# Optimization experiments

Measured on AMD Instinct MI355X. Metric: run time of the kernel, lower is better.

The kernel has to match this reference:

```python
import jax, jax.numpy as jnp
import numpy as np

N_EMBD = 384
NUM_HEADS = 6
HEAD_SIZE = 64
B, T = 64, 256


def setup_inputs() -> dict:
    key = jax.random.key(0)
    ks = jax.random.split(key, 6)
    s = 0.02
    x = jax.random.normal(ks[0], (B, T, N_EMBD), dtype=jnp.float32)
    # per-head projection weights, stored as [H, in, out] so y = x @ W
    Wq = jax.random.normal(ks[1], (NUM_HEADS, N_EMBD, HEAD_SIZE), dtype=jnp.float32) * s
    Wk = jax.random.normal(ks[2], (NUM_HEADS, N_EMBD, HEAD_SIZE), dtype=jnp.float32) * s
    Wv = jax.random.normal(ks[3], (NUM_HEADS, N_EMBD, HEAD_SIZE), dtype=jnp.float32) * s
    Wp = jax.random.normal(ks[4], (NUM_HEADS * HEAD_SIZE, N_EMBD), dtype=jnp.float32) * s
    bp = jax.random.normal(ks[5], (N_EMBD,), dtype=jnp.float32) * s
    return {"x": x, "Wq": Wq, "Wk": Wk, "Wv": Wv, "Wp": Wp, "bp": bp}


def reference(x, Wq, Wk, Wv, Wp, bp):
    # x: [B,T,C]; W{q,k,v}: [H,C,D]; dropout is identity (eval mode)
    Bb, Tt, _ = x.shape
    q = jnp.einsum('btc,hcd->bhtd', x, Wq)
    k = jnp.einsum('btc,hcd->bhtd', x, Wk)
    v = jnp.einsum('btc,hcd->bhtd', x, Wv)
    scale = HEAD_SIZE ** -0.5
    scores = jnp.einsum('bhtd,bhsd->bhts', q, k) * scale  # [B,H,T,T]
    causal = jnp.tril(jnp.ones((Tt, Tt), dtype=bool))
    scores = jnp.where(causal, scores, jnp.finfo(scores.dtype).min)
    attn = jax.nn.softmax(scores, axis=-1)
    out = jnp.einsum('bhts,bhsd->bhtd', attn, v)  # [B,H,T,D]
    out = out.transpose(0, 2, 1, 3).reshape(Bb, Tt, NUM_HEADS * HEAD_SIZE)
    return out @ Wp + bp
```

## Files before the change

### kernel.cpp

```cpp
#include <hip/hip_runtime.h>
#include <stdint.h>

#define B_  64
#define T_  256
#define C_  384
#define H_  6
#define D_  64
#define NTOK (B_*T_)

typedef float f32x4 __attribute__((ext_vector_type(4)));
typedef short s16x8 __attribute__((ext_vector_type(8)));

__device__ __forceinline__ unsigned short f2bf(float f) {
    unsigned int u;
    __builtin_memcpy(&u, &f, 4);
    u = u + 0x7FFFu + ((u >> 16) & 1u);
    return (unsigned short)(u >> 16);
}

__device__ __forceinline__ void async_copy16(const unsigned short* g, unsigned short* l) {
    __builtin_amdgcn_global_load_lds(
        (const __attribute__((address_space(1))) unsigned int*)g,
        (__attribute__((address_space(3))) unsigned int*)l, 16, 0, 0);
}

__global__ __launch_bounds__(256) void transpose_weights(
    const float* __restrict__ Wq, const float* __restrict__ Wk,
    const float* __restrict__ Wv, const float* __restrict__ Wp,
    unsigned short* __restrict__ W3, unsigned short* __restrict__ WTp) {
    __shared__ float tile[32][33];
    int z = blockIdx.y;
    const float* in;
    unsigned short* out;
    int R, Cc;
    if (z < 18) {
        int proj = z / 6, h = z % 6;
        const float* Wsrc = proj == 0 ? Wq : (proj == 1 ? Wk : Wv);
        in = Wsrc + h * C_ * D_;
        out = W3 + (size_t)(h * 192 + proj * 64) * C_;
        R = C_; Cc = D_;
    } else {
        in = Wp; out = WTp; R = C_; Cc = C_;
    }
    int tilesC = Cc / 32;
    int tilesR = R / 32;
    int bx = blockIdx.x;
    if (bx >= tilesC * tilesR) return;
    int tr = bx / tilesC, tc = bx % tilesC;
    int tx = threadIdx.x & 31;
    int ty8 = threadIdx.x >> 5;
    int gx = tc * 32 + tx;
#pragma unroll
    for (int i = 0; i < 4; i++) {
        int gy = tr * 32 + ty8 + i * 8;
        tile[ty8 + i * 8][tx] = in[gy * Cc + gx];
    }
    __syncthreads();
#pragma unroll
    for (int i = 0; i < 4; i++) {
        int oy = tc * 32 + ty8 + i * 8;
        int ox = tr * 32 + tx;
        out[oy * R + ox] = f2bf(tile[tx][ty8 + i * 8]);
    }
}

__global__ __launch_bounds__(512, 2) void fused_attn(
    const float* __restrict__ X, const unsigned short* __restrict__ W3,
    unsigned short* __restrict__ Ows) {
    __shared__ alignas(16) unsigned short smem[67584];
    unsigned short* Wc     = smem;
    unsigned short* q_lds  = smem + 18432;
    unsigned short* k_lds  = q_lds + 16384;
    unsigned short* vT_lds = k_lds + 16384;

    int bh = blockIdx.x;
    int h = bh >> 6, b = bh & 63;
    int tid = threadIdx.x;
    int w = tid >> 6, lane = tid & 63;
    int n16 = lane & 15, q4 = lane >> 4;
    const int jt[2] = {w, 15 - w};

    const unsigned short* W3h = W3 + (size_t)h * 192 * C_;
    const float* xb = X + (size_t)b * T_ * C_;

    f32x4 acc[2][12];
#pragma unroll
    for (int i = 0; i < 2; i++)
#pragma unroll
        for (int j = 0; j < 12; j++) acc[i][j] = (f32x4){0.f, 0.f, 0.f, 0.f};

    for (int kc = 0; kc < 4; kc++) {
        int ko = kc * 96;
        float4 a0[2][3], a1[2][3];
#pragma unroll
        for (int mi = 0; mi < 2; mi++)
#pragma unroll
            for (int ks = 0; ks < 3; ks++) {
                const float* ap = xb + (size_t)(jt[mi] * 16 + n16) * C_ + ko + ks * 32 + q4 * 8;
                a0[mi][ks] = *reinterpret_cast<const float4*>(ap);
                a1[mi][ks] = *reinterpret_cast<const float4*>(ap + 4);
            }
        if (kc) __syncthreads();
#pragma unroll
        for (int i = 0; i < 5; i++) {
            int sb = i * 512 + w * 64;
            if (sb < 2304) {
                int L = sb + lane;
                int row = L / 12;
                int c = L % 12;
                int ks = c >> 2;
                int q4g = (c & 3) ^ (row & 3);
                async_copy16(W3h + (size_t)row * C_ + ko + ks * 32 + q4g * 8,
                             Wc + (size_t)sb * 8);
            }
        }
        __syncthreads();
#pragma unroll
        for (int ks = 0; ks < 3; ks++) {
            s16x8 af[2];
#pragma unroll
            for (int mi = 0; mi < 2; mi++) {
                float4 lo = a0[mi][ks], hi = a1[mi][ks];
                s16x8 a;
                a[0] = (short)f2bf(lo.x); a[1] = (short)f2bf(lo.y);
                a[2] = (short)f2bf(lo.z); a[3] = (short)f2bf(lo.w);
                a[4] = (short)f2bf(hi.x); a[5] = (short)f2bf(hi.y);
                a[6] = (short)f2bf(hi.z); a[7] = (short)f2bf(hi.w);
                af[mi] = a;
            }
#pragma unroll
            for (int ni = 0; ni < 12; ni++) {
                int row = ni * 16 + n16;
                int cp = ks * 4 + (q4 ^ (row & 3));
                s16x8 bf = *reinterpret_cast<const s16x8*>(&Wc[row * 96 + cp * 8]);
                if (ni < 8) {
                    acc[0][ni] = __builtin_amdgcn_mfma_f32_16x16x32_bf16(bf, af[0], acc[0][ni], 0, 0, 0);
                    acc[1][ni] = __builtin_amdgcn_mfma_f32_16x16x32_bf16(bf, af[1], acc[1][ni], 0, 0, 0);
                } else {
                    acc[0][ni] = __builtin_amdgcn_mfma_f32_16x16x32_bf16(af[0], bf, acc[0][ni], 0, 0, 0);
                    acc[1][ni] = __builtin_amdgcn_mfma_f32_16x16x32_bf16(af[1], bf, acc[1][ni], 0, 0, 0);
                }
            }
        }
    }
#pragma unroll
    for (int mi = 0; mi < 2; mi++) {
        int tile = jt[mi];
#pragma unroll
        for (int ni = 0; ni < 12; ni++) {
            ushort4 pk;
            pk.x = f2bf(acc[mi][ni][0]); pk.y = f2bf(acc[mi][ni][1]);
            pk.z = f2bf(acc[mi][ni][2]); pk.w = f2bf(acc[mi][ni][3]);
            if (ni < 8) {
                int t = tile * 16 + n16;
                int cp = (2 * (ni & 3) + (q4 >> 1)) ^ (n16 & 7);
                unsigned short* dst = (ni < 4) ? q_lds : k_lds;
                *reinterpret_cast<ushort4*>(&dst[t * 64 + cp * 8 + (q4 & 1) * 4]) = pk;
            } else {
                int d = (ni - 8) * 16 + n16;
                int cp = (tile * 2 + (q4 >> 1)) ^ (d & 7);
                *reinterpret_cast<ushort4*>(&vT_lds[d * 256 + cp * 8 + (q4 & 1) * 4]) = pk;
            }
        }
    }
    __syncthreads();

    unsigned short* pw_base = smem + w * 1280;
    const f32x4 zero4 = (f32x4){0.f, 0.f, 0.f, 0.f};

#pragma unroll
    for (int tt = 0; tt < 2; tt++) {
        int j = jt[tt];
        int t0 = j * 16;
        int tq = t0 + n16;
        s16x8 qa0 = *reinterpret_cast<const s16x8*>(&q_lds[tq * 64 + ((q4 ^ (n16 & 7)) * 8)]);
        s16x8 qa1 = *reinterpret_cast<const s16x8*>(&q_lds[tq * 64 + (((q4 + 4) ^ (n16 & 7)) * 8)]);

        f32x4 o[4];
        float l_lane[4];
#pragma unroll
        for (int i = 0; i < 4; i++) o[i] = zero4;
#pragma unroll
        for (int r = 0; r < 4; r++) l_lane[r] = 0.f;

        int nch = j / 2 + 1;
        for (int c = 0; c < nch; c++) {
            int s0 = c * 32;
            bool bAct = (s0 + 16) < (t0 + 16);
            int r0 = s0 + n16, r1 = s0 + 16 + n16;
            s16x8 k00 = *reinterpret_cast<const s16x8*>(&k_lds[r0 * 64 + ((q4 ^ (r0 & 7)) * 8)]);
            s16x8 k01 = *reinterpret_cast<const s16x8*>(&k_lds[r0 * 64 + (((q4 + 4) ^ (r0 & 7)) * 8)]);
            f32x4 sv0 = __builtin_amdgcn_mfma_f32_16x16x32_bf16(qa0, k00, zero4, 0, 0, 0);
            sv0 = __builtin_amdgcn_mfma_f32_16x16x32_bf16(qa1, k01, sv0, 0, 0, 0);
            f32x4 sv1 = zero4;
            if (bAct) {
                s16x8 k10 = *reinterpret_cast<const s16x8*>(&k_lds[r1 * 64 + ((q4 ^ (r1 & 7)) * 8)]);
                s16x8 k11 = *reinterpret_cast<const s16x8*>(&k_lds[r1 * 64 + (((q4 + 4) ^ (r1 & 7)) * 8)]);
                sv1 = __builtin_amdgcn_mfma_f32_16x16x32_bf16(qa0, k10, zero4, 0, 0, 0);
                sv1 = __builtin_amdgcn_mfma_f32_16x16x32_bf16(qa1, k11, sv1, 0, 0, 0);
            }
            unsigned short* pw = pw_base + (c & 1) * 640;
#pragma unroll
            for (int r = 0; r < 4; r++) {
                int t = t0 + q4 * 4 + r;
                float pA = (s0 + n16 <= t) ? __expf(sv0[r] * 0.125f) : 0.f;
                float pB = (bAct && (s0 + 16 + n16 <= t)) ? __expf(sv1[r] * 0.125f) : 0.f;
                l_lane[r] += pA + pB;
                pw[(q4 * 4 + r) * 40 + n16] = f2bf(pA);
                pw[(q4 * 4 + r) * 40 + 16 + n16] = f2bf(pB);
            }
            s16x8 pa = *reinterpret_cast<const s16x8*>(&pw[n16 * 40 + q4 * 8]);
#pragma unroll
            for (int dt = 0; dt < 4; dt++) {
                int d = dt * 16 + n16;
                int jp = (c * 4 + q4) ^ (d & 7);
                s16x8 vf = *reinterpret_cast<const s16x8*>(&vT_lds[d * 256 + jp * 8]);
                o[dt] = __builtin_amdgcn_mfma_f32_16x16x32_bf16(pa, vf, o[dt], 0, 0, 0);
            }
        }

        float linv[4];
#pragma unroll
        for (int r = 0; r < 4; r++) {
            float l = l_lane[r];
            l += __shfl_xor(l, 1);
            l += __shfl_xor(l, 2);
            l += __shfl_xor(l, 4);
            l += __shfl_xor(l, 8);
            linv[r] = 1.0f / l;
        }
#pragma unroll
        for (int dt = 0; dt < 4; dt++) {
            int col = h * 64 + dt * 16 + n16;
#pragma unroll
            for (int r = 0; r < 4; r++)
                Ows[(size_t)(b * T_ + t0 + q4 * 4 + r) * C_ + col] = f2bf(o[dt][r] * linv[r]);
        }
    }
}

__global__ __launch_bounds__(256) void gemm_out(
    const unsigned short* __restrict__ A, const unsigned short* __restrict__ WTp,
    const float* __restrict__ bp, float* __restrict__ out) {
    __shared__ alignas(16) unsigned short Bt[6 * 128 * 32];
    int m0 = blockIdx.x * 128;
    int n0 = blockIdx.y * 128;
    int tid = threadIdx.x;
    int w = tid >> 6, lane = tid & 63;
    int n16 = lane & 15, q4 = lane >> 4;

    f32x4 acc[2][8];
#pragma unroll
    for (int i = 0; i < 2; i++)
#pragma unroll
        for (int j = 0; j < 8; j++) acc[i][j] = (f32x4){0.f, 0.f, 0.f, 0.f};

    const unsigned short* a_base[2];
#pragma unroll
    for (int mi = 0; mi < 2; mi++)
        a_base[mi] = A + (size_t)(m0 + w * 32 + mi * 16 + n16) * C_ + q4 * 8;

    for (int half = 0; half < 2; half++) {
        int ko = half * 192;
        s16x8 af[2][6];
#pragma unroll
        for (int mi = 0; mi < 2; mi++)
#pragma unroll
            for (int ks = 0; ks < 6; ks++)
                af[mi][ks] = *reinterpret_cast<const s16x8*>(a_base[mi] + ko + ks * 32);
        if (half) __syncthreads();
#pragma unroll
        for (int i = 0; i < 12; i++) {
            int L = w * 768 + i * 64 + lane;
            int kstep = L >> 9;
            int rem = L & 511;
            int row = rem >> 2;
            int j = (rem & 3) ^ (row & 3);
            async_copy16(WTp + (size_t)(n0 + row) * C_ + ko + kstep * 32 + j * 8,
                         Bt + (size_t)(w * 768 + i * 64) * 8);
        }
        __syncthreads();
#pragma unroll
        for (int ks = 0; ks < 6; ks++) {
            s16x8 bf[8];
#pragma unroll
            for (int ni = 0; ni < 8; ni++) {
                int row = ni * 16 + n16;
                int jp = q4 ^ (row & 3);
                bf[ni] = *reinterpret_cast<const s16x8*>(&Bt[ks * 4096 + row * 32 + jp * 8]);
            }
#pragma unroll
            for (int mi = 0; mi < 2; mi++)
#pragma unroll
                for (int ni = 0; ni < 8; ni++)
                    acc[mi][ni] = __builtin_amdgcn_mfma_f32_16x16x32_bf16(
                        bf[ni], af[mi][ks], acc[mi][ni], 0, 0, 0);
        }
    }

#pragma unroll
    for (int mi = 0; mi < 2; mi++) {
        int tr = m0 + w * 32 + mi * 16 + n16;
#pragma unroll
        for (int ni = 0; ni < 8; ni++) {
            int c0 = n0 + ni * 16 + q4 * 4;
            float4 bias = *reinterpret_cast<const float4*>(&bp[c0]);
            float4 res;
            res.x = acc[mi][ni][0] + bias.x;
            res.y = acc[mi][ni][1] + bias.y;
            res.z = acc[mi][ni][2] + bias.z;
            res.w = acc[mi][ni][3] + bias.w;
            *reinterpret_cast<float4*>(&out[(size_t)tr * C_ + c0]) = res;
        }
    }
}

extern "C" void kernel_launch(void* const* d_in, const int* in_sizes, int n_in,
                              void* d_out, int out_size, void* d_ws, size_t ws_size,
                              hipStream_t stream) {
    const float* x  = (const float*)d_in[0];
    const float* Wq = (const float*)d_in[1];
    const float* Wk = (const float*)d_in[2];
    const float* Wv = (const float*)d_in[3];
    const float* Wp = (const float*)d_in[4];
    const float* bp = (const float*)d_in[5];
    float* out = (float*)d_out;

    char* ws = (char*)d_ws;
    size_t off = 0;
    auto alloc = [&](size_t bytes) -> unsigned short* {
        unsigned short* p = (unsigned short*)(ws + off);
        off += (bytes + 255) & ~(size_t)255;
        return p;
    };
    unsigned short* W3  = alloc((size_t)H_ * 192 * C_ * 2);
    unsigned short* WTp = alloc((size_t)C_ * C_ * 2);
    unsigned short* Ows = alloc((size_t)NTOK * C_ * 2);

    transpose_weights<<<dim3(144, 19), dim3(256), 0, stream>>>(
        Wq, Wk, Wv, Wp, W3, WTp);
    fused_attn<<<dim3(B_ * H_), dim3(512), 0, stream>>>(x, W3, Ows);
    gemm_out<<<dim3(128, 3), dim3(256), 0, stream>>>(Ows, WTp, bp, out);
}
```

Measured before the change: 149.8 us.

## Double fused attention block to 16 waves with one query tile per wave

```diff
diff --git a/kernel.cpp b/kernel.cpp
--- a/kernel.cpp
+++ b/kernel.cpp
@@ -64,7 +64,7 @@
     }
 }
 
-__global__ __launch_bounds__(512, 2) void fused_attn(
+__global__ __launch_bounds__(1024, 4) void fused_attn(
     const float* __restrict__ X, const unsigned short* __restrict__ W3,
     unsigned short* __restrict__ Ows) {
     __shared__ alignas(16) unsigned short smem[67584];
@@ -78,32 +78,28 @@
     int tid = threadIdx.x;
     int w = tid >> 6, lane = tid & 63;
     int n16 = lane & 15, q4 = lane >> 4;
-    const int jt[2] = {w, 15 - w};
+    const int j = (w & 1) ? (15 - (w >> 1)) : (w >> 1);
 
     const unsigned short* W3h = W3 + (size_t)h * 192 * C_;
     const float* xb = X + (size_t)b * T_ * C_;
 
-    f32x4 acc[2][12];
-#pragma unroll
-    for (int i = 0; i < 2; i++)
-#pragma unroll
-        for (int j = 0; j < 12; j++) acc[i][j] = (f32x4){0.f, 0.f, 0.f, 0.f};
+    f32x4 acc[12];
+#pragma unroll
+    for (int i = 0; i < 12; i++) acc[i] = (f32x4){0.f, 0.f, 0.f, 0.f};
 
     for (int kc = 0; kc < 4; kc++) {
         int ko = kc * 96;
-        float4 a0[2][3], a1[2][3];
-#pragma unroll
-        for (int mi = 0; mi < 2; mi++)
-#pragma unroll
-            for (int ks = 0; ks < 3; ks++) {
-                const float* ap = xb + (size_t)(jt[mi] * 16 + n16) * C_ + ko + ks * 32 + q4 * 8;
-                a0[mi][ks] = *reinterpret_cast<const float4*>(ap);
-                a1[mi][ks] = *reinterpret_cast<const float4*>(ap + 4);
-            }
+        float4 a0[3], a1[3];
+#pragma unroll
+        for (int ks = 0; ks < 3; ks++) {
+            const float* ap = xb + (size_t)(j * 16 + n16) * C_ + ko + ks * 32 + q4 * 8;
+            a0[ks] = *reinterpret_cast<const float4*>(ap);
+            a1[ks] = *reinterpret_cast<const float4*>(ap + 4);
+        }
         if (kc) __syncthreads();
 #pragma unroll
-        for (int i = 0; i < 5; i++) {
-            int sb = i * 512 + w * 64;
+        for (int i = 0; i < 3; i++) {
+            int sb = i * 1024 + w * 64;
             if (sb < 2304) {
                 int L = sb + lane;
                 int row = L / 12;
@@ -117,60 +113,47 @@
         __syncthreads();
 #pragma unroll
         for (int ks = 0; ks < 3; ks++) {
-            s16x8 af[2];
-#pragma unroll
-            for (int mi = 0; mi < 2; mi++) {
-                float4 lo = a0[mi][ks], hi = a1[mi][ks];
-                s16x8 a;
-                a[0] = (short)f2bf(lo.x); a[1] = (short)f2bf(lo.y);
-                a[2] = (short)f2bf(lo.z); a[3] = (short)f2bf(lo.w);
-                a[4] = (short)f2bf(hi.x); a[5] = (short)f2bf(hi.y);
-                a[6] = (short)f2bf(hi.z); a[7] = (short)f2bf(hi.w);
-                af[mi] = a;
-            }
+            float4 lo = a0[ks], hi = a1[ks];
+            s16x8 af;
+            af[0] = (short)f2bf(lo.x); af[1] = (short)f2bf(lo.y);
+            af[2] = (short)f2bf(lo.z); af[3] = (short)f2bf(lo.w);
+            af[4] = (short)f2bf(hi.x); af[5] = (short)f2bf(hi.y);
+            af[6] = (short)f2bf(hi.z); af[7] = (short)f2bf(hi.w);
 #pragma unroll
             for (int ni = 0; ni < 12; ni++) {
                 int row = ni * 16 + n16;
                 int cp = ks * 4 + (q4 ^ (row & 3));
                 s16x8 bf = *reinterpret_cast<const s16x8*>(&Wc[row * 96 + cp * 8]);
                 if (ni < 8) {
-                    acc[0][ni] = __builtin_amdgcn_mfma_f32_16x16x32_bf16(bf, af[0], acc[0][ni], 0, 0, 0);
-                    acc[1][ni] = __builtin_amdgcn_mfma_f32_16x16x32_bf16(bf, af[1], acc[1][ni], 0, 0, 0);
+                    acc[ni] = __builtin_amdgcn_mfma_f32_16x16x32_bf16(bf, af, acc[ni], 0, 0, 0);
                 } else {
-                    acc[0][ni] = __builtin_amdgcn_mfma_f32_16x16x32_bf16(af[0], bf, acc[0][ni], 0, 0, 0);
-                    acc[1][ni] = __builtin_amdgcn_mfma_f32_16x16x32_bf16(af[1], bf, acc[1][ni], 0, 0, 0);
+                    acc[ni] = __builtin_amdgcn_mfma_f32_16x16x32_bf16(af, bf, acc[ni], 0, 0, 0);
                 }
             }
         }
     }
 #pragma unroll
-    for (int mi = 0; mi < 2; mi++) {
-        int tile = jt[mi];
-#pragma unroll
-        for (int ni = 0; ni < 12; ni++) {
-            ushort4 pk;
-            pk.x = f2bf(acc[mi][ni][0]); pk.y = f2bf(acc[mi][ni][1]);
-            pk.z = f2bf(acc[mi][ni][2]); pk.w = f2bf(acc[mi][ni][3]);
-            if (ni < 8) {
-                int t = tile * 16 + n16;
-                int cp = (2 * (ni & 3) + (q4 >> 1)) ^ (n16 & 7);
-                unsigned short* dst = (ni < 4) ? q_lds : k_lds;
-                *reinterpret_cast<ushort4*>(&dst[t * 64 + cp * 8 + (q4 & 1) * 4]) = pk;
-            } else {
-                int d = (ni - 8) * 16 + n16;
-                int cp = (tile * 2 + (q4 >> 1)) ^ (d & 7);
-                *reinterpret_cast<ushort4*>(&vT_lds[d * 256 + cp * 8 + (q4 & 1) * 4]) = pk;
-            }
+    for (int ni = 0; ni < 12; ni++) {
+        ushort4 pk;
+        pk.x = f2bf(acc[ni][0]); pk.y = f2bf(acc[ni][1]);
+        pk.z = f2bf(acc[ni][2]); pk.w = f2bf(acc[ni][3]);
+        if (ni < 8) {
+            int t = j * 16 + n16;
+            int cp = (2 * (ni & 3) + (q4 >> 1)) ^ (n16 & 7);
+            unsigned short* dst = (ni < 4) ? q_lds : k_lds;
+            *reinterpret_cast<ushort4*>(&dst[t * 64 + cp * 8 + (q4 & 1) * 4]) = pk;
+        } else {
+            int d = (ni - 8) * 16 + n16;
+            int cp = (j * 2 + (q4 >> 1)) ^ (d & 7);
+            *reinterpret_cast<ushort4*>(&vT_lds[d * 256 + cp * 8 + (q4 & 1) * 4]) = pk;
         }
     }
     __syncthreads();
 
-    unsigned short* pw_base = smem + w * 1280;
+    unsigned short* pw = smem + w * 640;
     const f32x4 zero4 = (f32x4){0.f, 0.f, 0.f, 0.f};
 
-#pragma unroll
-    for (int tt = 0; tt < 2; tt++) {
-        int j = jt[tt];
+    {
         int t0 = j * 16;
         int tq = t0 + n16;
         s16x8 qa0 = *reinterpret_cast<const s16x8*>(&q_lds[tq * 64 + ((q4 ^ (n16 & 7)) * 8)]);
@@ -199,7 +182,6 @@
                 sv1 = __builtin_amdgcn_mfma_f32_16x16x32_bf16(qa0, k10, zero4, 0, 0, 0);
                 sv1 = __builtin_amdgcn_mfma_f32_16x16x32_bf16(qa1, k11, sv1, 0, 0, 0);
             }
-            unsigned short* pw = pw_base + (c & 1) * 640;
 #pragma unroll
             for (int r = 0; r < 4; r++) {
                 int t = t0 + q4 * 4 + r;
@@ -339,6 +321,6 @@
 
     transpose_weights<<<dim3(144, 19), dim3(256), 0, stream>>>(
         Wq, Wk, Wv, Wp, W3, WTp);
-    fused_attn<<<dim3(B_ * H_), dim3(512), 0, stream>>>(x, W3, Ows);
+    fused_attn<<<dim3(B_ * H_), dim3(1024), 0, stream>>>(x, W3, Ows);
     gemm_out<<<dim3(128, 3), dim3(256), 0, stream>>>(Ows, WTp, bp, out);
 }
```

New measurement: 151.6 us. No clear change (+1.2%).

## Double attention block threads and read projection weights directly from global

Applied to the files above, without the earlier changes.

```diff
diff --git a/kernel.cpp b/kernel.cpp
--- a/kernel.cpp
+++ b/kernel.cpp
@@ -8,8 +8,8 @@
 #define D_  64
 #define NTOK (B_*T_)
 
-typedef float f32x4 __attribute__((ext_vector_type(4)));
-typedef short s16x8 __attribute__((ext_vector_type(8)));
+typedef float f32x4  __attribute__((ext_vector_type(4)));
+typedef short s16x8  __attribute__((ext_vector_type(8)));
 
 __device__ __forceinline__ unsigned short f2bf(float f) {
     unsigned int u;
@@ -64,11 +64,10 @@
     }
 }
 
-__global__ __launch_bounds__(512, 2) void fused_attn(
+__global__ __launch_bounds__(1024, 4) void fused_attn(
     const float* __restrict__ X, const unsigned short* __restrict__ W3,
     unsigned short* __restrict__ Ows) {
     __shared__ alignas(16) unsigned short smem[67584];
-    unsigned short* Wc     = smem;
     unsigned short* q_lds  = smem + 18432;
     unsigned short* k_lds  = q_lds + 16384;
     unsigned short* vT_lds = k_lds + 16384;
@@ -78,16 +77,19 @@
     int tid = threadIdx.x;
     int w = tid >> 6, lane = tid & 63;
     int n16 = lane & 15, q4 = lane >> 4;
-    const int jt[2] = {w, 15 - w};
+    int p = w >> 1, hh = w & 1;
+    const int jt[2] = {p, 15 - p};
+    const int ni0 = hh * 6;
+    const int j = (w & 1) ? (15 - (w >> 1)) : (w >> 1);
 
     const unsigned short* W3h = W3 + (size_t)h * 192 * C_;
     const float* xb = X + (size_t)b * T_ * C_;
 
-    f32x4 acc[2][12];
+    f32x4 acc[2][6];
 #pragma unroll
     for (int i = 0; i < 2; i++)
 #pragma unroll
-        for (int j = 0; j < 12; j++) acc[i][j] = (f32x4){0.f, 0.f, 0.f, 0.f};
+        for (int jj = 0; jj < 6; jj++) acc[i][jj] = (f32x4){0.f, 0.f, 0.f, 0.f};
 
     for (int kc = 0; kc < 4; kc++) {
         int ko = kc * 96;
@@ -100,21 +102,6 @@
                 a0[mi][ks] = *reinterpret_cast<const float4*>(ap);
                 a1[mi][ks] = *reinterpret_cast<const float4*>(ap + 4);
             }
-        if (kc) __syncthreads();
-#pragma unroll
-        for (int i = 0; i < 5; i++) {
-            int sb = i * 512 + w * 64;
-            if (sb < 2304) {
-                int L = sb + lane;
-                int row = L / 12;
-                int c = L % 12;
-                int ks = c >> 2;
-                int q4g = (c & 3) ^ (row & 3);
-                async_copy16(W3h + (size_t)row * C_ + ko + ks * 32 + q4g * 8,
-                             Wc + (size_t)sb * 8);
-            }
-        }
-        __syncthreads();
 #pragma unroll
         for (int ks = 0; ks < 3; ks++) {
             s16x8 af[2];
@@ -129,16 +116,17 @@
                 af[mi] = a;
             }
 #pragma unroll
-            for (int ni = 0; ni < 12; ni++) {
+            for (int i = 0; i < 6; i++) {
+                int ni = ni0 + i;
                 int row = ni * 16 + n16;
-                int cp = ks * 4 + (q4 ^ (row & 3));
-                s16x8 bf = *reinterpret_cast<const s16x8*>(&Wc[row * 96 + cp * 8]);
+                s16x8 bf = *reinterpret_cast<const s16x8*>(
+                    W3h + (size_t)row * C_ + ko + ks * 32 + q4 * 8);
                 if (ni < 8) {
-                    acc[0][ni] = __builtin_amdgcn_mfma_f32_16x16x32_bf16(bf, af[0], acc[0][ni], 0, 0, 0);
-                    acc[1][ni] = __builtin_amdgcn_mfma_f32_16x16x32_bf16(bf, af[1], acc[1][ni], 0, 0, 0);
+                    acc[0][i] = __builtin_amdgcn_mfma_f32_16x16x32_bf16(bf, af[0], acc[0][i], 0, 0, 0);
+                    acc[1][i] = __builtin_amdgcn_mfma_f32_16x16x32_bf16(bf, af[1], acc[1][i], 0, 0, 0);
                 } else {
-                    acc[0][ni] = __builtin_amdgcn_mfma_f32_16x16x32_bf16(af[0], bf, acc[0][ni], 0, 0, 0);
-                    acc[1][ni] = __builtin_amdgcn_mfma_f32_16x16x32_bf16(af[1], bf, acc[1][ni], 0, 0, 0);
+                    acc[0][i] = __builtin_amdgcn_mfma_f32_16x16x32_bf16(af[0], bf, acc[0][i], 0, 0, 0);
+                    acc[1][i] = __builtin_amdgcn_mfma_f32_16x16x32_bf16(af[1], bf, acc[1][i], 0, 0, 0);
                 }
             }
         }
@@ -147,10 +135,11 @@
     for (int mi = 0; mi < 2; mi++) {
         int tile = jt[mi];
 #pragma unroll
-        for (int ni = 0; ni < 12; ni++) {
+        for (int i = 0; i < 6; i++) {
+            int ni = ni0 + i;
             ushort4 pk;
-            pk.x = f2bf(acc[mi][ni][0]); pk.y = f2bf(acc[mi][ni][1]);
-            pk.z = f2bf(acc[mi][ni][2]); pk.w = f2bf(acc[mi][ni][3]);
+            pk.x = f2bf(acc[mi][i][0]); pk.y = f2bf(acc[mi][i][1]);
+            pk.z = f2bf(acc[mi][i][2]); pk.w = f2bf(acc[mi][i][3]);
             if (ni < 8) {
                 int t = tile * 16 + n16;
                 int cp = (2 * (ni & 3) + (q4 >> 1)) ^ (n16 & 7);
@@ -165,12 +154,10 @@
     }
     __syncthreads();
 
-    unsigned short* pw_base = smem + w * 1280;
+    unsigned short* pw = smem + w * 640;
     const f32x4 zero4 = (f32x4){0.f, 0.f, 0.f, 0.f};
 
-#pragma unroll
-    for (int tt = 0; tt < 2; tt++) {
-        int j = jt[tt];
+    {
         int t0 = j * 16;
         int tq = t0 + n16;
         s16x8 qa0 = *reinterpret_cast<const s16x8*>(&q_lds[tq * 64 + ((q4 ^ (n16 & 7)) * 8)]);
@@ -199,7 +186,6 @@
                 sv1 = __builtin_amdgcn_mfma_f32_16x16x32_bf16(qa0, k10, zero4, 0, 0, 0);
                 sv1 = __builtin_amdgcn_mfma_f32_16x16x32_bf16(qa1, k11, sv1, 0, 0, 0);
             }
-            unsigned short* pw = pw_base + (c & 1) * 640;
 #pragma unroll
             for (int r = 0; r < 4; r++) {
                 int t = t0 + q4 * 4 + r;
@@ -339,6 +325,6 @@
 
     transpose_weights<<<dim3(144, 19), dim3(256), 0, stream>>>(
         Wq, Wk, Wv, Wp, W3, WTp);
-    fused_attn<<<dim3(B_ * H_), dim3(512), 0, stream>>>(x, W3, Ows);
+    fused_attn<<<dim3(B_ * H_), dim3(1024), 0, stream>>>(x, W3, Ows);
     gemm_out<<<dim3(128, 3), dim3(256), 0, stream>>>(Ows, WTp, bp, out);
 }
```

Result: slower. 228.2 us (+52.3%).

## Shrink LDS footprint to raise occupancy: narrower K chunks, Q in registers

Applied to the files above, without the earlier changes.

```diff
diff --git a/kernel.cpp b/kernel.cpp
--- a/kernel.cpp
+++ b/kernel.cpp
@@ -8,8 +8,8 @@
 #define D_  64
 #define NTOK (B_*T_)
 
-typedef float f32x4 __attribute__((ext_vector_type(4)));
-typedef short s16x8 __attribute__((ext_vector_type(8)));
+typedef float f32x4  __attribute__((ext_vector_type(4)));
+typedef short s16x8  __attribute__((ext_vector_type(8)));
 
 __device__ __forceinline__ unsigned short f2bf(float f) {
     unsigned int u;
@@ -64,13 +64,12 @@
     }
 }
 
-__global__ __launch_bounds__(512, 2) void fused_attn(
+__global__ __launch_bounds__(512, 4) void fused_attn(
     const float* __restrict__ X, const unsigned short* __restrict__ W3,
     unsigned short* __restrict__ Ows) {
-    __shared__ alignas(16) unsigned short smem[67584];
+    __shared__ alignas(16) unsigned short smem[38912];
     unsigned short* Wc     = smem;
-    unsigned short* q_lds  = smem + 18432;
-    unsigned short* k_lds  = q_lds + 16384;
+    unsigned short* k_lds  = smem + 6144;
     unsigned short* vT_lds = k_lds + 16384;
 
     int bh = blockIdx.x;
@@ -87,62 +86,66 @@
 #pragma unroll
     for (int i = 0; i < 2; i++)
 #pragma unroll
-        for (int j = 0; j < 12; j++) acc[i][j] = (f32x4){0.f, 0.f, 0.f, 0.f};
-
-    for (int kc = 0; kc < 4; kc++) {
-        int ko = kc * 96;
-        float4 a0[2][3], a1[2][3];
-#pragma unroll
-        for (int mi = 0; mi < 2; mi++)
-#pragma unroll
-            for (int ks = 0; ks < 3; ks++) {
-                const float* ap = xb + (size_t)(jt[mi] * 16 + n16) * C_ + ko + ks * 32 + q4 * 8;
-                a0[mi][ks] = *reinterpret_cast<const float4*>(ap);
-                a1[mi][ks] = *reinterpret_cast<const float4*>(ap + 4);
-            }
+        for (int jj = 0; jj < 12; jj++) acc[i][jj] = (f32x4){0.f, 0.f, 0.f, 0.f};
+
+    float4 a0[2], a1[2];
+#pragma unroll
+    for (int mi = 0; mi < 2; mi++) {
+        const float* ap = xb + (size_t)(jt[mi] * 16 + n16) * C_ + q4 * 8;
+        a0[mi] = *reinterpret_cast<const float4*>(ap);
+        a1[mi] = *reinterpret_cast<const float4*>(ap + 4);
+    }
+
+    for (int kc = 0; kc < 12; kc++) {
+        int ko = kc * 32;
         if (kc) __syncthreads();
-#pragma unroll
-        for (int i = 0; i < 5; i++) {
-            int sb = i * 512 + w * 64;
-            if (sb < 2304) {
-                int L = sb + lane;
-                int row = L / 12;
-                int c = L % 12;
-                int ks = c >> 2;
-                int q4g = (c & 3) ^ (row & 3);
-                async_copy16(W3h + (size_t)row * C_ + ko + ks * 32 + q4g * 8,
-                             Wc + (size_t)sb * 8);
+        {
+            int L = w * 64 + lane;
+            int row = L >> 2, c = L & 3;
+            async_copy16(W3h + (size_t)row * C_ + ko + ((c ^ (row & 3)) * 8),
+                         Wc + (size_t)L * 8);
+            if (w < 4) {
+                int L2 = 512 + w * 64 + lane;
+                int row2 = L2 >> 2, c2 = L2 & 3;
+                async_copy16(W3h + (size_t)row2 * C_ + ko + ((c2 ^ (row2 & 3)) * 8),
+                             Wc + (size_t)L2 * 8);
             }
         }
         __syncthreads();
-#pragma unroll
-        for (int ks = 0; ks < 3; ks++) {
-            s16x8 af[2];
+        s16x8 af[2];
+#pragma unroll
+        for (int mi = 0; mi < 2; mi++) {
+            float4 lo = a0[mi], hi = a1[mi];
+            s16x8 a;
+            a[0] = (short)f2bf(lo.x); a[1] = (short)f2bf(lo.y);
+            a[2] = (short)f2bf(lo.z); a[3] = (short)f2bf(lo.w);
+            a[4] = (short)f2bf(hi.x); a[5] = (short)f2bf(hi.y);
+            a[6] = (short)f2bf(hi.z); a[7] = (short)f2bf(hi.w);
+            af[mi] = a;
+        }
+        if (kc < 11) {
 #pragma unroll
             for (int mi = 0; mi < 2; mi++) {
-                float4 lo = a0[mi][ks], hi = a1[mi][ks];
-                s16x8 a;
-                a[0] = (short)f2bf(lo.x); a[1] = (short)f2bf(lo.y);
-                a[2] = (short)f2bf(lo.z); a[3] = (short)f2bf(lo.w);
-                a[4] = (short)f2bf(hi.x); a[5] = (short)f2bf(hi.y);
-                a[6] = (short)f2bf(hi.z); a[7] = (short)f2bf(hi.w);
-                af[mi] = a;
-            }
-#pragma unroll
-            for (int ni = 0; ni < 12; ni++) {
-                int row = ni * 16 + n16;
-                int cp = ks * 4 + (q4 ^ (row & 3));
-                s16x8 bf = *reinterpret_cast<const s16x8*>(&Wc[row * 96 + cp * 8]);
-                if (ni < 8) {
-                    acc[0][ni] = __builtin_amdgcn_mfma_f32_16x16x32_bf16(bf, af[0], acc[0][ni], 0, 0, 0);
-                    acc[1][ni] = __builtin_amdgcn_mfma_f32_16x16x32_bf16(bf, af[1], acc[1][ni], 0, 0, 0);
-                } else {
-                    acc[0][ni] = __builtin_amdgcn_mfma_f32_16x16x32_bf16(af[0], bf, acc[0][ni], 0, 0, 0);
-                    acc[1][ni] = __builtin_amdgcn_mfma_f32_16x16x32_bf16(af[1], bf, acc[1][ni], 0, 0, 0);
-                }
-            }
-        }
-    }
+                const float* ap = xb + (size_t)(jt[mi] * 16 + n16) * C_ + (ko + 32) + q4 * 8;
+                a0[mi] = *reinterpret_cast<const float4*>(ap);
+                a1[mi] = *reinterpret_cast<const float4*>(ap + 4);
+            }
+        }
+#pragma unroll
+        for (int ni = 0; ni < 12; ni++) {
+            int row = ni * 16 + n16;
+            s16x8 bf = *reinterpret_cast<const s16x8*>(&Wc[row * 32 + ((q4 ^ (row & 3)) * 8)]);
+            if (ni < 8) {
+                acc[0][ni] = __builtin_amdgcn_mfma_f32_16x16x32_bf16(bf, af[0], acc[0][ni], 0, 0, 0);
+                acc[1][ni] = __builtin_amdgcn_mfma_f32_16x16x32_bf16(bf, af[1], acc[1][ni], 0, 0, 0);
+            } else {
+                acc[0][ni] = __builtin_amdgcn_mfma_f32_16x16x32_bf16(af[0], bf, acc[0][ni], 0, 0, 0);
+                acc[1][ni] = __builtin_amdgcn_mfma_f32_16x16x32_bf16(af[1], bf, acc[1][ni], 0, 0, 0);
+            }
+        }
+    }
+
+    unsigned int qd[2][4][2];
 #pragma unroll
     for (int mi = 0; mi < 2; mi++) {
         int tile = jt[mi];
@@ -151,11 +154,13 @@
             ushort4 pk;
             pk.x = f2bf(acc[mi][ni][0]); pk.y = f2bf(acc[mi][ni][1]);
             pk.z = f2bf(acc[mi][ni][2]); pk.w = f2bf(acc[mi][ni][3]);
-            if (ni < 8) {
+            if (ni < 4) {
+                qd[mi][ni][0] = (unsigned int)pk.x | ((unsigned int)pk.y << 16);
+                qd[mi][ni][1] = (unsigned int)pk.z | ((unsigned int)pk.w << 16);
+            } else if (ni < 8) {
                 int t = tile * 16 + n16;
                 int cp = (2 * (ni & 3) + (q4 >> 1)) ^ (n16 & 7);
-                unsigned short* dst = (ni < 4) ? q_lds : k_lds;
-                *reinterpret_cast<ushort4*>(&dst[t * 64 + cp * 8 + (q4 & 1) * 4]) = pk;
+                *reinterpret_cast<ushort4*>(&k_lds[t * 64 + cp * 8 + (q4 & 1) * 4]) = pk;
             } else {
                 int d = (ni - 8) * 16 + n16;
                 int cp = (tile * 2 + (q4 >> 1)) ^ (d & 7);
@@ -163,18 +168,48 @@
             }
         }
     }
+
+    s16x8 qa[2][2];
+    {
+        int addrA = (n16 + 32 * (q4 & 1)) * 4;
+        int addrB = addrA + 64;
+        bool hi = (q4 & 2) != 0;
+#pragma unroll
+        for (int mi = 0; mi < 2; mi++) {
+#pragma unroll
+            for (int half = 0; half < 2; half++) {
+                unsigned int s0x = qd[mi][half * 2][0],     s0y = qd[mi][half * 2][1];
+                unsigned int s1x = qd[mi][half * 2 + 1][0], s1y = qd[mi][half * 2 + 1][1];
+                unsigned int A0x = (unsigned int)__builtin_amdgcn_ds_bpermute(addrA, (int)s0x);
+                unsigned int A1x = (unsigned int)__builtin_amdgcn_ds_bpermute(addrA, (int)s1x);
+                unsigned int A0y = (unsigned int)__builtin_amdgcn_ds_bpermute(addrA, (int)s0y);
+                unsigned int A1y = (unsigned int)__builtin_amdgcn_ds_bpermute(addrA, (int)s1y);
+                unsigned int B0x = (unsigned int)__builtin_amdgcn_ds_bpermute(addrB, (int)s0x);
+                unsigned int B1x = (unsigned int)__builtin_amdgcn_ds_bpermute(addrB, (int)s1x);
+                unsigned int B0y = (unsigned int)__builtin_amdgcn_ds_bpermute(addrB, (int)s0y);
+                unsigned int B1y = (unsigned int)__builtin_amdgcn_ds_bpermute(addrB, (int)s1y);
+                unsigned int t[4];
+                t[0] = hi ? A1x : A0x;
+                t[1] = hi ? A1y : A0y;
+                t[2] = hi ? B1x : B0x;
+                t[3] = hi ? B1y : B0y;
+                s16x8 q;
+                __builtin_memcpy(&q, t, 16);
+                qa[mi][half] = q;
+            }
+        }
+    }
     __syncthreads();
 
-    unsigned short* pw_base = smem + w * 1280;
+    unsigned short* pw = smem + w * 640;
     const f32x4 zero4 = (f32x4){0.f, 0.f, 0.f, 0.f};
 
 #pragma unroll
     for (int tt = 0; tt < 2; tt++) {
         int j = jt[tt];
         int t0 = j * 16;
-        int tq = t0 + n16;
-        s16x8 qa0 = *reinterpret_cast<const s16x8*>(&q_lds[tq * 64 + ((q4 ^ (n16 & 7)) * 8)]);
-        s16x8 qa1 = *reinterpret_cast<const s16x8*>(&q_lds[tq * 64 + (((q4 + 4) ^ (n16 & 7)) * 8)]);
+        s16x8 qa0 = qa[tt][0];
+        s16x8 qa1 = qa[tt][1];
 
         f32x4 o[4];
         float l_lane[4];
@@ -199,7 +234,6 @@
                 sv1 = __builtin_amdgcn_mfma_f32_16x16x32_bf16(qa0, k10, zero4, 0, 0, 0);
                 sv1 = __builtin_amdgcn_mfma_f32_16x16x32_bf16(qa1, k11, sv1, 0, 0, 0);
             }
-            unsigned short* pw = pw_base + (c & 1) * 640;
 #pragma unroll
             for (int r = 0; r < 4; r++) {
                 int t = t0 + q4 * 4 + r;
```

New measurement: 145.4 us (median of 2 runs). -3.0%, faster.
